# Kernel optimization log

Hardware: AMD Instinct MI355X
Metric: run time of the kernel (lower is better)

## Reference

```python
import jax, jax.numpy as jnp
import numpy as np
import math

D_MODEL = 1024
N_HEADS = 16
D_KV = 64
ROPE_BASE = 10000.0


def absmean_quantize_weight(w):
    # ternary absmean quantization: scale = mean(|w|), round-to-nearest-even, clamp to {-1,0,1}
    scale = jnp.mean(jnp.abs(w))
    return jnp.clip(jnp.round(w / scale), -1.0, 1.0) * scale


def quantize_activation(x, num_bits=8):
    qmax = 2.0 ** (num_bits - 1) - 1.0  # 127
    scale = jnp.max(jnp.abs(x)) / qmax
    return jnp.clip(jnp.round(x / scale), -qmax, qmax) * scale


def bitlinear(x, w):
    return quantize_activation(x) @ absmean_quantize_weight(w).T


def rope_tables(seq_len, dim, dtype):
    inv_freq = 1.0 / (ROPE_BASE ** (jnp.arange(0, dim, 2, dtype=jnp.float32) / dim))
    t = jnp.arange(seq_len, dtype=jnp.float32)
    freqs = jnp.einsum('i,j->ij', t, inv_freq)        # [S, dim/2]
    emb = jnp.concatenate([freqs, freqs], axis=-1)    # [S, dim]
    # broadcast shape [1, 1, S, dim]
    return jnp.cos(emb)[None, None].astype(dtype), jnp.sin(emb)[None, None].astype(dtype)


def rotate_half(x):
    x1, x2 = jnp.split(x, 2, axis=-1)
    return jnp.concatenate([-x2, x1], axis=-1)


def setup_inputs() -> dict:
    key = jax.random.key(0)
    ks = jax.random.split(key, 5)
    B, S = 2, 2048
    bound = 1.0 / math.sqrt(D_MODEL)  # kaiming-uniform-ish scale
    return {
        'hidden_states': jax.random.normal(ks[0], (B, S, D_MODEL), dtype=jnp.float32),
        'Wq': jax.random.uniform(ks[1], (N_HEADS * D_KV, D_MODEL), jnp.float32, -bound, bound),
        'Wk': jax.random.uniform(ks[2], (N_HEADS * D_KV, D_MODEL), jnp.float32, -bound, bound),
        'Wv': jax.random.uniform(ks[3], (N_HEADS * D_KV, D_MODEL), jnp.float32, -bound, bound),
        'Wo': jax.random.uniform(ks[4], (D_MODEL, N_HEADS * D_KV), jnp.float32, -bound, bound),
    }


def reference(hidden_states, Wq, Wk, Wv, Wo):
    B, S, _ = hidden_states.shape
    inner = N_HEADS * D_KV

    def split_heads(x):
        return x.reshape(B, S, N_HEADS, D_KV).transpose(0, 2, 1, 3)  # [B,H,S,Dk]

    q = split_heads(bitlinear(hidden_states, Wq))
    k = split_heads(bitlinear(hidden_states, Wk))
    v = split_heads(bitlinear(hidden_states, Wv))

    cos, sin = rope_tables(S, D_KV, q.dtype)
    q = q * cos + rotate_half(q) * sin
    k = k * cos + rotate_half(k) * sin

    scores = jnp.einsum('bhqd,bhkd->bhqk', q, k) / math.sqrt(D_KV)
    attn_weights = jax.nn.softmax(scores.astype(jnp.float32), axis=-1).astype(scores.dtype)
    # dropout p=0.0 / eval mode -> identity
    attn_output = jnp.einsum('bhqk,bhkd->bhqd', attn_weights, v)
    attn_output = attn_output.transpose(0, 2, 1, 3).reshape(B, S, inner)
    attn_output = bitlinear(attn_output, Wo)
    return attn_output, attn_weights
```

## Files before the change

### kernel.cpp

```cpp
#include <hip/hip_runtime.h>
#include <math.h>

typedef __attribute__((ext_vector_type(8))) short short8;
typedef __attribute__((ext_vector_type(4))) float f32x4;
typedef __attribute__((ext_vector_type(4))) int i32x4;
typedef __attribute__((ext_vector_type(4))) unsigned int u32x4;

#define DEV __device__ __forceinline__

static constexpr int B_ = 2, S_ = 2048, H_ = 16, D_ = 64, DM_ = 1024;
static constexpr int BH_ = B_ * H_;
static constexpr int NQ_ = B_ * S_;
static constexpr size_t OUT0_ELEMS = (size_t)NQ_ * DM_;
static constexpr float LOG2E = 1.4426950408889634f;
static constexpr float A2 = 0.125f * 1.4426950408889634f;

static constexpr size_t OFF_PMAXX = 256;
static constexpr size_t OFF_PSUM  = 1280;
static constexpr size_t OFF_PMAXA = 4096;
static constexpr size_t OFF_K2M   = 12288;
static constexpr size_t OFF_COS   = 16384;
static constexpr size_t OFF_SIN   = OFF_COS + (size_t)S_ * 32 * 4;
static constexpr size_t OFF_Q2    = OFF_SIN + (size_t)S_ * 32 * 4;
static constexpr size_t OFF_XQ    = (size_t)1 << 20;
static constexpr size_t OFF_WQ8   = OFF_XQ   + (size_t)NQ_ * DM_;
static constexpr size_t OFF_QB    = OFF_WQ8  + (size_t)4096 * 1024;
static constexpr size_t OFF_KB    = OFF_QB   + (size_t)BH_ * S_ * D_ * 2;
static constexpr size_t OFF_VT    = OFF_KB   + (size_t)BH_ * S_ * D_ * 2;
static constexpr size_t OFF_APRE  = OFF_VT   + (size_t)BH_ * D_ * S_ * 2;
static constexpr size_t OFF_AQ    = OFF_APRE + (size_t)NQ_ * DM_ * 4;
static constexpr size_t WS_NEED   = OFF_AQ   + (size_t)NQ_ * DM_;

DEV unsigned short f2bf(float f) {
  unsigned u = __builtin_bit_cast(unsigned, f);
  return (unsigned short)((u + 0x7fffu + ((u >> 16) & 1u)) >> 16);
}
DEV float bf2f(unsigned short h) {
  unsigned u = ((unsigned)h) << 16;
  return __builtin_bit_cast(float, u);
}
DEV void gload16(const void* g, void* l) {
  __builtin_amdgcn_global_load_lds((const __attribute__((address_space(1))) unsigned int*)g,
                                   (__attribute__((address_space(3))) unsigned int*)l, 16, 0, 0);
}
DEV int q8pack(float4 v, float sc, float lim) {
  int i0 = (int)fminf(fmaxf(rintf(v.x / sc), -lim), lim);
  int i1 = (int)fminf(fmaxf(rintf(v.y / sc), -lim), lim);
  int i2 = (int)fminf(fmaxf(rintf(v.z / sc), -lim), lim);
  int i3 = (int)fminf(fmaxf(rintf(v.w / sc), -lim), lim);
  return (int)(((unsigned)(i0 & 255)) | ((unsigned)(i1 & 255) << 8) |
               ((unsigned)(i2 & 255) << 16) | ((unsigned)(i3 & 255) << 24));
}

__global__ void k_reduce6(const float* __restrict__ x, const float* __restrict__ w0,
                          const float* __restrict__ w1, const float* __restrict__ w2,
                          const float* __restrict__ w3, float* __restrict__ pmaxx,
                          float* __restrict__ psum, float* __restrict__ cosT,
                          float* __restrict__ sinT) {
  __shared__ float red[256];
  const int y = blockIdx.y;
  if (y == 5) {
    const int i0 = (blockIdx.x * 256 + threadIdx.x) * 2;
#pragma unroll
    for (int t = 0; t < 2; ++t) {
      const int i = i0 + t;
      const int s = i >> 5, f = i & 31;
      double inv = pow(10000.0, -(double)(2 * f) / 64.0);
      float th = (float)s * (float)inv;
      cosT[i] = (float)cos((double)th);
      sinT[i] = (float)sin((double)th);
    }
    return;
  }
  if (y == 0) {
    const float4* xv = (const float4*)x;
    float mv = 0.f;
    for (int i = blockIdx.x * 256 + threadIdx.x; i < 1048576; i += 128 * 256) {
      float4 v = xv[i];
      mv = fmaxf(mv, fmaxf(fmaxf(fabsf(v.x), fabsf(v.y)), fmaxf(fabsf(v.z), fabsf(v.w))));
    }
    red[threadIdx.x] = mv;
    __syncthreads();
    for (int st = 128; st > 0; st >>= 1) {
      if ((int)threadIdx.x < st) red[threadIdx.x] = fmaxf(red[threadIdx.x], red[threadIdx.x + st]);
      __syncthreads();
    }
    if (threadIdx.x == 0) pmaxx[blockIdx.x] = red[0];
  } else {
    const float* wsrc = (y == 1) ? w0 : (y == 2) ? w1 : (y == 3) ? w2 : w3;
    const float4* xv = (const float4*)wsrc;
    float s = 0.f;
    for (int i = blockIdx.x * 256 + threadIdx.x; i < 262144; i += 128 * 256) {
      float4 v = xv[i];
      s += fabsf(v.x) + fabsf(v.y) + fabsf(v.z) + fabsf(v.w);
    }
    red[threadIdx.x] = s;
    __syncthreads();
    for (int st = 128; st > 0; st >>= 1) {
      if ((int)threadIdx.x < st) red[threadIdx.x] += red[threadIdx.x + st];
      __syncthreads();
    }
    if (threadIdx.x == 0) psum[(y - 1) * 128 + blockIdx.x] = red[0];
  }
}

__global__ void k_finalize1(float* __restrict__ wsf, float* __restrict__ k2m) {
  const float* pmax = wsf + OFF_PMAXX / 4;
  const float* psum = wsf + OFF_PSUM / 4;
  const int w = threadIdx.x >> 6, l = threadIdx.x & 63;
  float s = psum[w * 128 + l] + psum[w * 128 + 64 + l];
#pragma unroll
  for (int off = 1; off < 64; off <<= 1) s += __shfl_xor(s, off);
  if (l == 0) wsf[1 + w] = s / 1048576.0f;
  if (w == 0) {
    float m = fmaxf(pmax[l], pmax[l + 64]);
#pragma unroll
    for (int off = 1; off < 64; off <<= 1) m = fmaxf(m, __shfl_xor(m, off));
    if (l == 0) wsf[0] = m / 127.0f;
  }
  if (threadIdx.x < 32) k2m[threadIdx.x] = 0.f;
}

__global__ void k_quant_all(const float* __restrict__ x, const float* __restrict__ w0,
                            const float* __restrict__ w1, const float* __restrict__ w2,
                            const float* __restrict__ w3, const float* __restrict__ scal,
                            signed char* __restrict__ xq, signed char* __restrict__ wq) {
  const int bid = blockIdx.x;
  if (bid < 4096) {
    const int i = bid * 256 + threadIdx.x;
    const float sc = scal[0];
    ((int*)xq)[i] = q8pack(((const float4*)x)[i], sc, 127.f);
  } else {
    const int wi = bid - 4096;
    const int y = wi >> 10;
    const int i = (wi & 1023) * 256 + threadIdx.x;
    const float* src = (y == 0) ? w0 : (y == 1) ? w1 : (y == 2) ? w2 : w3;
    const float sc = scal[1 + y];
    ((int*)(wq + (size_t)y * 1048576))[i] = q8pack(((const float4*)src)[i], sc, 1.f);
  }
}

__global__ void k_quant_a8(const float* __restrict__ x, const float* __restrict__ pmaxa,
                           float* __restrict__ wsf, signed char* __restrict__ out) {
  __shared__ float red[256];
  float m = 0.f;
  for (int k = threadIdx.x; k < 1024; k += 256) m = fmaxf(m, pmaxa[k]);
  red[threadIdx.x] = m;
  __syncthreads();
  for (int st = 128; st > 0; st >>= 1) {
    if ((int)threadIdx.x < st) red[threadIdx.x] = fmaxf(red[threadIdx.x], red[threadIdx.x + st]);
    __syncthreads();
  }
  const float sc = red[0] / 127.0f;
  if (blockIdx.x == 0 && threadIdx.x == 0) wsf[5] = sc;
  const int i = blockIdx.x * 256 + threadIdx.x;
  ((int*)out)[i] = q8pack(((const float4*)x)[i], sc, 127.f);
}

template <int MODE>
__launch_bounds__(256, 3)
__global__ void k_gemm(const signed char* __restrict__ Ag, const signed char* __restrict__ Bg,
                       const float* __restrict__ scal, const float* __restrict__ cosT,
                       const float* __restrict__ sinT, unsigned short* __restrict__ Qb,
                       unsigned short* __restrict__ Kb, unsigned short* __restrict__ Vt,
                       float* __restrict__ q2t, float* __restrict__ k2m, float* __restrict__ Co) {
  constexpr int TM = (MODE == 0) ? 128 : 64;
  constexpr int MT = TM / 32;
  __shared__ alignas(16) unsigned char As[3][TM * 64];
  __shared__ alignas(16) unsigned char Bs[3][128 * 64];
  const int w = threadIdx.x >> 6, l = threadIdx.x & 63;
  const int mbase = blockIdx.y * TM, nbase = blockIdx.x * 128;

  const i32x4 izero = {0, 0, 0, 0};
  i32x4 acc[MT][4];
#pragma unroll
  for (int a = 0; a < MT; ++a)
#pragma unroll
    for (int b = 0; b < 4; ++b) acc[a][b] = izero;

  const int csrc = (l & 3) ^ ((l >> 2) & 3) ^ ((l >> 4) & 3);
  const int r16 = l >> 2;

  auto stage = [&](int kt, int buf) {
#pragma unroll
    for (int i = 0; i < TM / 64; ++i) {
      const int chunk = w * (TM / 64) + i;
      const int grow = mbase + chunk * 16 + r16;
      gload16(Ag + (size_t)grow * 1024 + kt * 64 + csrc * 16, &As[buf][chunk << 10]);
    }
#pragma unroll
    for (int i = 0; i < 2; ++i) {
      const int chunk = w * 2 + i;
      const int grow = nbase + chunk * 16 + r16;
      gload16(Bg + (size_t)grow * 1024 + kt * 64 + csrc * 16, &Bs[buf][chunk << 10]);
    }
  };
  auto wait_lps = [&]() {
    if constexpr (MODE == 0) asm volatile("s_waitcnt vmcnt(4)" ::: "memory");
    else asm volatile("s_waitcnt vmcnt(3)" ::: "memory");
  };

  const int rA0 = (w >> 1) * (TM / 2) + (l & 15);
  const int rB0 = (w & 1) * 64 + (l & 15);
  const int kc = l >> 4;
  auto compute = [&](int buf) {
    const unsigned char* Ab = &As[buf][0];
    const unsigned char* Bb = &Bs[buf][0];
    i32x4 af[MT], bf[4];
#pragma unroll
    for (int t = 0; t < MT; ++t) {
      const int ra = rA0 + t * 16;
      af[t] = *(const i32x4*)(Ab + ra * 64 + ((kc ^ (ra & 3) ^ ((ra >> 2) & 3)) << 4));
    }
#pragma unroll
    for (int t = 0; t < 4; ++t) {
      const int rb = rB0 + t * 16;
      bf[t] = *(const i32x4*)(Bb + rb * 64 + ((kc ^ (rb & 3) ^ ((rb >> 2) & 3)) << 4));
    }
#pragma unroll
    for (int mt = 0; mt < MT; ++mt)
#pragma unroll
      for (int nt = 0; nt < 4; ++nt)
        acc[mt][nt] = __builtin_amdgcn_mfma_i32_16x16x64_i8(af[mt], bf[nt], acc[mt][nt], 0, 0, 0);
  };

  stage(0, 0);
  stage(1, 1);
  wait_lps();
  __syncthreads();
  for (int kt = 0; kt < 16; ++kt) {
    const int cur = kt % 3;
    if (kt < 14) {
      stage(kt + 2, (kt + 2) % 3);
      compute(cur);
      wait_lps();
    } else {
      compute(cur);
      asm volatile("s_waitcnt vmcnt(0)" ::: "memory");
    }
    __syncthreads();
  }

  if constexpr (MODE == 0) {
    const int wm = w >> 1, wn = w & 1;
    const int gcolbase = nbase + wn * 64;
    const int section = gcolbase >> 10;
    const int h = (gcolbase & 1023) >> 6;
    const float sc = scal[0] * scal[1 + section];
    const int growbase = mbase + wm * 64;
    if (section < 2) {
      unsigned short* Outb = (section == 0) ? Qb : Kb;
      float wmax = 0.f;
#pragma unroll
      for (int mt = 0; mt < MT; ++mt)
#pragma unroll
        for (int r = 0; r < 4; ++r) {
          const int grow = growbase + mt * 16 + ((l >> 4) << 2) + r;
          const int b = grow >> 11, s = grow & 2047;
          const size_t ob = ((size_t)(b * 16 + h) * 2048 + s) * 64;
          float rsq = 0.f;
#pragma unroll
          for (int nt = 0; nt < 2; ++nt) {
            const int d = nt * 16 + (l & 15);
            const float v1 = (float)acc[mt][nt][r] * sc;
            const float v2 = (float)acc[mt][nt + 2][r] * sc;
            const float cv = cosT[s * 32 + d];
            const float sv = sinT[s * 32 + d];
            const unsigned short h1 = f2bf(v1 * cv - v2 * sv);
            const unsigned short h2 = f2bf(v2 * cv + v1 * sv);
            Outb[ob + d] = h1;
            Outb[ob + d + 32] = h2;
            const float o1 = bf2f(h1), o2 = bf2f(h2);
            rsq += o1 * o1 + o2 * o2;
          }
#pragma unroll
          for (int off = 1; off < 16; off <<= 1) rsq += __shfl_xor(rsq, off);
          if (section == 0) {
            if ((l & 15) == 0) q2t[(size_t)(b * 16 + h) * 2048 + s] = rsq;
          } else {
            wmax = fmaxf(wmax, rsq);
          }
        }
      if (section == 1) {
        wmax = fmaxf(wmax, __shfl_xor(wmax, 16));
        wmax = fmaxf(wmax, __shfl_xor(wmax, 32));
        if (l == 0) {
          const int b = growbase >> 11;
          atomicMax((unsigned int*)&k2m[b * 16 + h], __builtin_bit_cast(unsigned int, wmax));
        }
      }
    } else {
      const int bh = (growbase >> 11) * 16 + h;
      unsigned short* Tw = (unsigned short*)(&As[0][0]) + w * 2176;
#pragma unroll
      for (int h0 = 0; h0 < 2; ++h0) {
#pragma unroll
        for (int mh = 0; mh < 2; ++mh) {
          const int mt = h0 * 2 + mh;
#pragma unroll
          for (int r = 0; r < 4; ++r) {
            const int srow = mh * 16 + ((l >> 4) << 2) + r;
#pragma unroll
            for (int nt = 0; nt < 4; ++nt)
              Tw[srow * 68 + nt * 16 + (l & 15)] = f2bf((float)acc[mt][nt][r] * sc);
          }
        }
        asm volatile("s_waitcnt lgkmcnt(0)" ::: "memory");
        __builtin_amdgcn_sched_barrier(0);
        const int i = l & 15, dq = l >> 4;
#pragma unroll
        for (int d0 = 0; d0 < 16; ++d0) {
          const int d = d0 * 4 + dq;
          const unsigned a = Tw[(2 * i) * 68 + d];
          const unsigned b2 = Tw[(2 * i + 1) * 68 + d];
          const int sglob = growbase + h0 * 32 + 2 * i;
          const int b = sglob >> 11, s = sglob & 2047;
          *(unsigned*)(Vt + ((size_t)((b * 16 + h) * 64 + d) * 2048 + s)) = a | (b2 << 16);
        }
        asm volatile("s_waitcnt lgkmcnt(0)" ::: "memory");
        __builtin_amdgcn_sched_barrier(0);
      }
    }
  } else {
    const float sc = scal[4] * scal[5];
#pragma unroll
    for (int mt = 0; mt < MT; ++mt)
#pragma unroll
      for (int r = 0; r < 4; ++r) {
        const int grow = mbase + (w >> 1) * (TM / 2) + mt * 16 + ((l >> 4) << 2) + r;
#pragma unroll
        for (int nt = 0; nt < 4; ++nt) {
          const int gcol = nbase + (w & 1) * 64 + nt * 16 + (l & 15);
          Co[(size_t)grow * 1024 + gcol] = (float)acc[mt][nt][r] * sc;
        }
      }
  }
}

__launch_bounds__(256, 3)
__global__ void k_attn(const unsigned short* __restrict__ Qb, const unsigned short* __restrict__ Kb,
                       const unsigned short* __restrict__ Vt, const float* __restrict__ q2t,
                       const float* __restrict__ k2m, float* __restrict__ Wout,
                       float* __restrict__ Apre, float* __restrict__ pmaxa) {
  __shared__ alignas(16) unsigned short Ks[2][64 * 64];
  __shared__ alignas(16) unsigned short Vhs[2][64 * 64];
  __shared__ alignas(16) float Ps[4][16 * 64];

  const int bid = (int)blockIdx.x;
  const int swz = ((bid & 7) << 7) | (bid >> 3);
  const int bh = swz >> 5, qt = swz & 31;
  const int w = threadIdx.x >> 6, l = threadIdx.x & 63;

  const unsigned short* Kg = Kb + (size_t)bh * S_ * D_;
  const unsigned short* Vg = Vt + (size_t)bh * D_ * S_;

  short8 aq[2];
  {
    const int qrow_f = qt * 64 + w * 16 + (l & 15);
    const unsigned short* qp = Qb + (size_t)bh * S_ * D_ + (size_t)qrow_f * D_ + ((l >> 4) << 3);
    aq[0] = *(const short8*)qp;
    aq[1] = *(const short8*)(qp + 32);
  }

  float cb[4];
  {
    const float km = k2m[bh];
#pragma unroll
    for (int r = 0; r < 4; ++r) {
      const int qr = qt * 64 + w * 16 + ((l >> 4) << 2) + r;
      cb[r] = sqrtf(q2t[(size_t)bh * 2048 + qr] * km) * 0.125f * LOG2E;
    }
  }

  const f32x4 vzero = {0.f, 0.f, 0.f, 0.f};
  const int kxor = ((l & 7) << 4) ^ ((l >> 3) << 4);
  const int lxor = ((l << 4) ^ ((l >> 3) << 4));

  auto stageK = [&](int kb, int buf) {
    const char* baseK = (const char*)(Kg + (size_t)kb * 64 * D_);
#pragma unroll
    for (int i = 0; i < 2; ++i) {
      int j = (w << 1) + i;
      gload16(baseK + (j << 10) + lxor, (char*)&Ks[buf][0] + (j << 10));
    }
  };
  auto stageB = [&](int kb, int buf) {
    const char* baseK = (const char*)(Kg + (size_t)kb * 64 * D_);
#pragma unroll
    for (int i = 0; i < 2; ++i) {
      int j = (w << 1) + i;
      gload16(baseK + (j << 10) + lxor, (char*)&Ks[buf][0] + (j << 10));
      const size_t voff = (size_t)(j * 8 + (l >> 3)) * (S_ * 2) + (size_t)kb * 128 + kxor;
      gload16((const char*)Vg + voff, (char*)&Vhs[buf][0] + (j << 10));
    }
  };
  auto qkt = [&](int buf, f32x4* sa) {
    const char* Kbase = (const char*)&Ks[buf][0];
#pragma unroll
    for (int c = 0; c < 2; ++c) {
      const int colb = (c << 6) + ((l >> 4) << 4);
      short8 bk[4];
#pragma unroll
      for (int ct = 0; ct < 4; ++ct) {
        const int rb = (ct << 4) + (l & 15);
        bk[ct] = *(const short8*)(Kbase + rb * 128 + (colb ^ ((rb & 7) << 4)));
      }
#pragma unroll
      for (int ct = 0; ct < 4; ++ct)
        sa[ct] = __builtin_amdgcn_mfma_f32_16x16x32_bf16(aq[c], bk[ct], sa[ct], 0, 0, 0);
    }
  };

  float lt[4] = {0.f, 0.f, 0.f, 0.f};
  stageK(0, 0);
  asm volatile("s_waitcnt vmcnt(0)" ::: "memory");
  __syncthreads();
  for (int kb = 0; kb < 32; ++kb) {
    const int cur = kb & 1;
    if (kb < 31) stageK(kb + 1, cur ^ 1);
    f32x4 sa[4];
#pragma unroll
    for (int t = 0; t < 4; ++t) sa[t] = vzero;
    qkt(cur, sa);
#pragma unroll
    for (int r = 0; r < 4; ++r) {
      lt[r] += exp2f(fmaf(sa[0][r], A2, -cb[r])) + exp2f(fmaf(sa[1][r], A2, -cb[r])) +
               exp2f(fmaf(sa[2][r], A2, -cb[r])) + exp2f(fmaf(sa[3][r], A2, -cb[r]));
    }
    asm volatile("s_waitcnt vmcnt(0)" ::: "memory");
    __syncthreads();
  }

  float rl[4];
#pragma unroll
  for (int r = 0; r < 4; ++r) {
    float s = lt[r];
#pragma unroll
    for (int off = 1; off < 16; off <<= 1) s += __shfl_xor(s, off);
    rl[r] = 1.0f / s;
  }

  f32x4 oacc[4];
#pragma unroll
  for (int t = 0; t < 4; ++t) oacc[t] = vzero;
  float* Pw = &Ps[w][0];
  const size_t wb0 = (size_t)bh * S_ * S_;

  stageB(0, 0);
  asm volatile("s_waitcnt vmcnt(0)" ::: "memory");
  __syncthreads();
  for (int kb = 0; kb < 32; ++kb) {
    const int cur = kb & 1;
    if (kb < 31) stageB(kb + 1, cur ^ 1);

    f32x4 sa[4];
#pragma unroll
    for (int t = 0; t < 4; ++t) sa[t] = vzero;
    qkt(cur, sa);

#pragma unroll
    for (int ct = 0; ct < 4; ++ct) {
#pragma unroll
      for (int r = 0; r < 4; ++r) {
        const float p = exp2f(fmaf(sa[ct][r], A2, -cb[r])) * rl[r];
        const int prow = ((l >> 4) << 2) + r;
        const int pbyte = (ct * 16 + (l & 15)) << 2;
        *(float*)((char*)Pw + prow * 256 + (pbyte ^ ((prow & 7) << 4))) = p;
      }
    }

    {
      const size_t wrow0 = wb0 + (size_t)(qt * 64 + w * 16) * S_ + (size_t)kb * 64;
#pragma unroll
      for (int i = 0; i < 4; ++i) {
        const int prow = (i << 2) + (l >> 4);
        const int cb2 = (l & 15) << 4;
        const f32x4 f = *(const f32x4*)((const char*)Pw + prow * 256 + (cb2 ^ ((prow & 7) << 4)));
        __builtin_nontemporal_store(
            f, (f32x4*)(Wout + wrow0 + (size_t)prow * S_ + ((l & 15) << 2)));
      }
    }

#pragma unroll
    for (int c = 0; c < 2; ++c) {
      const int arow = l & 15;
      const int abyte = (c << 7) + ((l >> 4) << 5);
      const u32x4 u0 = *(const u32x4*)((const char*)Pw + arow * 256 + (abyte ^ ((arow & 7) << 4)));
      const u32x4 u1 =
          *(const u32x4*)((const char*)Pw + arow * 256 + ((abyte + 16) ^ ((arow & 7) << 4)));
      short8 ph, pl;
#pragma unroll
      for (int j = 0; j < 4; ++j) {
        const unsigned ua = u0[j], ub = u1[j];
        ph[j] = (short)(ua >> 16);
        ph[4 + j] = (short)(ub >> 16);
        const float da = __builtin_bit_cast(float, ua) -
                         __builtin_bit_cast(float, ua & 0xffff0000u);
        const float db = __builtin_bit_cast(float, ub) -
                         __builtin_bit_cast(float, ub & 0xffff0000u);
        pl[j] = (short)(__builtin_bit_cast(unsigned, da) >> 16);
        pl[4 + j] = (short)(__builtin_bit_cast(unsigned, db) >> 16);
      }
      const int colb = (c << 6) + ((l >> 4) << 4);
#pragma unroll
      for (int dt = 0; dt < 4; ++dt) {
        const int rv = (dt << 4) + (l & 15);
        const short8 vh = *(const short8*)((const char*)&Vhs[cur][0] + rv * 128 + (colb ^ ((rv & 7) << 4)));
        oacc[dt] = __builtin_amdgcn_mfma_f32_16x16x32_bf16(ph, vh, oacc[dt], 0, 0, 0);
        oacc[dt] = __builtin_amdgcn_mfma_f32_16x16x32_bf16(pl, vh, oacc[dt], 0, 0, 0);
      }
    }
    asm volatile("s_waitcnt vmcnt(4)" ::: "memory");
    __syncthreads();
  }

  const int b = bh >> 4, h = bh & 15;
  float am = 0.f;
#pragma unroll
  for (int dt = 0; dt < 4; ++dt)
#pragma unroll
    for (int r = 0; r < 4; ++r) {
      const int qr = qt * 64 + w * 16 + ((l >> 4) << 2) + r;
      Apre[(size_t)(b * S_ + qr) * DM_ + h * 64 + dt * 16 + (l & 15)] = oacc[dt][r];
      am = fmaxf(am, fabsf(oacc[dt][r]));
    }
#pragma unroll
  for (int off = 1; off < 64; off <<= 1) am = fmaxf(am, __shfl_xor(am, off));
  __syncthreads();
  float* red = (float*)&Ps[0][0];
  if (l == 0) red[w] = am;
  __syncthreads();
  if (threadIdx.x == 0)
    pmaxa[bid] = fmaxf(fmaxf(red[0], red[1]), fmaxf(red[2], red[3]));
}

extern "C" void kernel_launch(void* const* d_in, const int* in_sizes, int n_in, void* d_out,
                              int out_size, void* d_ws, size_t ws_size, hipStream_t stream) {
  const float* hidden = (const float*)d_in[0];
  const float* Wq = (const float*)d_in[1];
  const float* Wk = (const float*)d_in[2];
  const float* Wv = (const float*)d_in[3];
  const float* Wo = (const float*)d_in[4];
  float* out0 = (float*)d_out;
  float* out1 = out0 + OUT0_ELEMS;

  if (ws_size < WS_NEED) return;

  char* ws = (char*)d_ws;
  float* wsf = (float*)ws;
  float* pmaxx = (float*)(ws + OFF_PMAXX);
  float* psum = (float*)(ws + OFF_PSUM);
  float* pmaxa = (float*)(ws + OFF_PMAXA);
  float* k2mp = (float*)(ws + OFF_K2M);
  float* cosT = (float*)(ws + OFF_COS);
  float* sinT = (float*)(ws + OFF_SIN);
  float* q2p = (float*)(ws + OFF_Q2);
  signed char* xq8 = (signed char*)(ws + OFF_XQ);
  signed char* wq8 = (signed char*)(ws + OFF_WQ8);
  unsigned short* Qbp = (unsigned short*)(ws + OFF_QB);
  unsigned short* Kbp = (unsigned short*)(ws + OFF_KB);
  unsigned short* Vtp = (unsigned short*)(ws + OFF_VT);
  float* apre = (float*)(ws + OFF_APRE);
  signed char* aq8 = (signed char*)(ws + OFF_AQ);

  k_reduce6<<<dim3(128, 6), 256, 0, stream>>>(hidden, Wq, Wk, Wv, Wo, pmaxx, psum, cosT, sinT);
  k_finalize1<<<1, 256, 0, stream>>>(wsf, k2mp);
  k_quant_all<<<8192, 256, 0, stream>>>(hidden, Wq, Wk, Wv, Wo, wsf, xq8, wq8);
  k_gemm<0><<<dim3(24, 32), 256, 0, stream>>>(xq8, wq8, wsf, cosT, sinT, Qbp, Kbp, Vtp, q2p, k2mp,
                                              nullptr);
  k_attn<<<1024, 256, 0, stream>>>(Qbp, Kbp, Vtp, q2p, k2mp, out1, apre, pmaxa);
  k_quant_a8<<<4096, 256, 0, stream>>>(apre, pmaxa, wsf, aq8);
  k_gemm<1><<<dim3(8, 64), 256, 0, stream>>>(aq8, wq8 + (size_t)3 * 1048576, wsf, nullptr, nullptr,
                                             nullptr, nullptr, nullptr, nullptr, nullptr, out0);
  (void)in_sizes; (void)n_in; (void)out_size;
}
```

Baseline: 253.1 us.

## Triple-buffer K loads in attention stats pass and swizzle GEMM block order

The attention kernel's first pass (row-sum of exponentials) now prefetches K tiles two iterations ahead using a three-slot ring buffer in a unified shared-memory arena, waiting with vmcnt(2) instead of draining all loads each iteration. The aliased arena keeps LDS footprint at 48KB. The GEMM kernels remap block indices with an 8-way interleave so consecutive blocks spread across tiles, aiming for better L2/XCD locality. The remap assumes exact grid dims (24 or 8 column blocks) and slightly adds integer math.

```diff
diff --git a/kernel.cpp b/kernel.cpp
--- a/kernel.cpp
+++ b/kernel.cpp
@@ -166,10 +166,15 @@
                        float* __restrict__ q2t, float* __restrict__ k2m, float* __restrict__ Co) {
   constexpr int TM = (MODE == 0) ? 128 : 64;
   constexpr int MT = TM / 32;
+  constexpr int NBX = (MODE == 0) ? 24 : 8;
+  constexpr int CPX = (MODE == 0) ? 96 : 64;
   __shared__ alignas(16) unsigned char As[3][TM * 64];
   __shared__ alignas(16) unsigned char Bs[3][128 * 64];
   const int w = threadIdx.x >> 6, l = threadIdx.x & 63;
-  const int mbase = blockIdx.y * TM, nbase = blockIdx.x * 128;
+
+  const int bid = (int)blockIdx.x + (int)blockIdx.y * NBX;
+  const int nl = (bid & 7) * CPX + (bid >> 3);
+  const int mbase = (nl / NBX) * TM, nbase = (nl % NBX) * 128;
 
   const i32x4 izero = {0, 0, 0, 0};
   i32x4 acc[MT][4];
@@ -290,7 +295,6 @@
         }
       }
     } else {
-      const int bh = (growbase >> 11) * 16 + h;
       unsigned short* Tw = (unsigned short*)(&As[0][0]) + w * 2176;
 #pragma unroll
       for (int h0 = 0; h0 < 2; ++h0) {
@@ -342,9 +346,7 @@
                        const unsigned short* __restrict__ Vt, const float* __restrict__ q2t,
                        const float* __restrict__ k2m, float* __restrict__ Wout,
                        float* __restrict__ Apre, float* __restrict__ pmaxa) {
-  __shared__ alignas(16) unsigned short Ks[2][64 * 64];
-  __shared__ alignas(16) unsigned short Vhs[2][64 * 64];
-  __shared__ alignas(16) float Ps[4][16 * 64];
+  __shared__ alignas(16) char smem[48 * 1024];
 
   const int bid = (int)blockIdx.x;
   const int swz = ((bid & 7) << 7) | (bid >> 3);
@@ -376,26 +378,15 @@
   const int kxor = ((l & 7) << 4) ^ ((l >> 3) << 4);
   const int lxor = ((l << 4) ^ ((l >> 3) << 4));
 
-  auto stageK = [&](int kb, int buf) {
+  auto stageKbuf = [&](int kb, char* dst) {
     const char* baseK = (const char*)(Kg + (size_t)kb * 64 * D_);
 #pragma unroll
     for (int i = 0; i < 2; ++i) {
       int j = (w << 1) + i;
-      gload16(baseK + (j << 10) + lxor, (char*)&Ks[buf][0] + (j << 10));
+      gload16(baseK + (j << 10) + lxor, dst + (j << 10));
     }
   };
-  auto stageB = [&](int kb, int buf) {
-    const char* baseK = (const char*)(Kg + (size_t)kb * 64 * D_);
-#pragma unroll
-    for (int i = 0; i < 2; ++i) {
-      int j = (w << 1) + i;
-      gload16(baseK + (j << 10) + lxor, (char*)&Ks[buf][0] + (j << 10));
-      const size_t voff = (size_t)(j * 8 + (l >> 3)) * (S_ * 2) + (size_t)kb * 128 + kxor;
-      gload16((const char*)Vg + voff, (char*)&Vhs[buf][0] + (j << 10));
-    }
-  };
-  auto qkt = [&](int buf, f32x4* sa) {
-    const char* Kbase = (const char*)&Ks[buf][0];
+  auto qktbuf = [&](const char* Kbase, f32x4* sa) {
 #pragma unroll
     for (int c = 0; c < 2; ++c) {
       const int colb = (c << 6) + ((l >> 4) << 4);
@@ -412,22 +403,27 @@
   };
 
   float lt[4] = {0.f, 0.f, 0.f, 0.f};
-  stageK(0, 0);
-  asm volatile("s_waitcnt vmcnt(0)" ::: "memory");
+  stageKbuf(0, smem);
+  stageKbuf(1, smem + 8192);
+  asm volatile("s_waitcnt vmcnt(2)" ::: "memory");
   __syncthreads();
   for (int kb = 0; kb < 32; ++kb) {
-    const int cur = kb & 1;
-    if (kb < 31) stageK(kb + 1, cur ^ 1);
+    const int cur = kb % 3;
+    if (kb < 30) stageKbuf(kb + 2, smem + ((kb + 2) % 3) * 8192);
     f32x4 sa[4];
 #pragma unroll
     for (int t = 0; t < 4; ++t) sa[t] = vzero;
-    qkt(cur, sa);
+    qktbuf(smem + cur * 8192, sa);
 #pragma unroll
     for (int r = 0; r < 4; ++r) {
       lt[r] += exp2f(fmaf(sa[0][r], A2, -cb[r])) + exp2f(fmaf(sa[1][r], A2, -cb[r])) +
                exp2f(fmaf(sa[2][r], A2, -cb[r])) + exp2f(fmaf(sa[3][r], A2, -cb[r]));
     }
-    asm volatile("s_waitcnt vmcnt(0)" ::: "memory");
+    if (kb < 31) {
+      asm volatile("s_waitcnt vmcnt(2)" ::: "memory");
+    } else {
+      asm volatile("s_waitcnt vmcnt(0)" ::: "memory");
+    }
     __syncthreads();
   }
 
@@ -443,8 +439,21 @@
   f32x4 oacc[4];
 #pragma unroll
   for (int t = 0; t < 4; ++t) oacc[t] = vzero;
-  float* Pw = &Ps[w][0];
+  char* KsB = smem;
+  char* VhsB = smem + 16384;
+  float* Pw = (float*)(smem + 32768) + w * 1024;
   const size_t wb0 = (size_t)bh * S_ * S_;
+
+  auto stageB = [&](int kb, int buf) {
+    const char* baseK = (const char*)(Kg + (size_t)kb * 64 * D_);
+#pragma unroll
+    for (int i = 0; i < 2; ++i) {
+      int j = (w << 1) + i;
+      gload16(baseK + (j << 10) + lxor, KsB + buf * 8192 + (j << 10));
+      const size_t voff = (size_t)(j * 8 + (l >> 3)) * (S_ * 2) + (size_t)kb * 128 + kxor;
+      gload16((const char*)Vg + voff, VhsB + buf * 8192 + (j << 10));
+    }
+  };
 
   stageB(0, 0);
   asm volatile("s_waitcnt vmcnt(0)" ::: "memory");
@@ -456,7 +465,7 @@
     f32x4 sa[4];
 #pragma unroll
     for (int t = 0; t < 4; ++t) sa[t] = vzero;
-    qkt(cur, sa);
+    qktbuf(KsB + cur * 8192, sa);
 
 #pragma unroll
     for (int ct = 0; ct < 4; ++ct) {
@@ -505,7 +514,8 @@
 #pragma unroll
       for (int dt = 0; dt < 4; ++dt) {
         const int rv = (dt << 4) + (l & 15);
-        const short8 vh = *(const short8*)((const char*)&Vhs[cur][0] + rv * 128 + (colb ^ ((rv & 7) << 4)));
+        const short8 vh =
+            *(const short8*)(VhsB + cur * 8192 + rv * 128 + (colb ^ ((rv & 7) << 4)));
         oacc[dt] = __builtin_amdgcn_mfma_f32_16x16x32_bf16(ph, vh, oacc[dt], 0, 0, 0);
         oacc[dt] = __builtin_amdgcn_mfma_f32_16x16x32_bf16(pl, vh, oacc[dt], 0, 0, 0);
       }
@@ -527,7 +537,7 @@
 #pragma unroll
   for (int off = 1; off < 64; off <<= 1) am = fmaxf(am, __shfl_xor(am, off));
   __syncthreads();
-  float* red = (float*)&Ps[0][0];
+  float* red = (float*)smem;
   if (l == 0) red[w] = am;
   __syncthreads();
   if (threadIdx.x == 0)
```

After: 223.4 us. 11.8% less time.
